# Optimization experiments

Measured on AMD Instinct MI355X. Metric: run time of the kernel, lower is better.

Reference implementation:

```python
import jax, jax.numpy as jnp
import numpy as np

NUM_USERS = 100000
NUM_ITEMS = 50000
N_NODES = NUM_USERS + NUM_ITEMS
LATENT_DIM = 64
XIJ_DIM = 16
N_LAYERS = 3
NNZ = 6400000
BATCH = 8192


def setup_inputs() -> dict:
    key = jax.random.key(0)
    ks = jax.random.split(key, 12)
    return {
        "emb_user": jax.random.normal(ks[0], (NUM_USERS, LATENT_DIM), jnp.float32),
        "emb_item": jax.random.normal(ks[1], (NUM_ITEMS, LATENT_DIM), jnp.float32),
        "emb_user_xij": jax.random.normal(ks[2], (NUM_USERS, XIJ_DIM), jnp.float32),
        "emb_item_xij1": jax.random.normal(ks[3], (NUM_ITEMS, XIJ_DIM), jnp.float32),
        "emb_item_xij0": jax.random.normal(ks[4], (NUM_ITEMS, XIJ_DIM), jnp.float32),
        "w_user": jax.random.normal(ks[5], (1,), jnp.float32),
        "w_item": jax.random.normal(ks[6], (1,), jnp.float32),
        "graph_vals": jax.random.uniform(ks[7], (NNZ,), jnp.float32),
        "graph_rows": jax.random.randint(ks[8], (NNZ,), 0, N_NODES, jnp.int64).astype(jnp.int32),
        "graph_cols": jax.random.randint(ks[9], (NNZ,), 0, N_NODES, jnp.int64).astype(jnp.int32),
        "users": jax.random.randint(ks[10], (BATCH,), 0, NUM_USERS, jnp.int64).astype(jnp.int32),
        "items": jax.random.randint(ks[11], (BATCH,), 0, NUM_ITEMS, jnp.int64).astype(jnp.int32),
        "xij": jax.random.randint(jax.random.fold_in(key, 99), (BATCH,), 0, 2, jnp.int32),
    }


def _spmm(rows, cols, vals, x):
    # y[r] = sum_{e: rows[e]==r} vals[e] * x[cols[e]]
    return jax.ops.segment_sum(vals[:, None] * x[cols], rows, num_segments=N_NODES)


def reference(emb_user, emb_item, emb_user_xij, emb_item_xij1, emb_item_xij0,
              w_user, w_item, graph_vals, graph_rows, graph_cols,
              users, items, xij):
    # LightGCN propagation with running-mean accumulator (fuses the stack+mean)
    all_emb = jnp.concatenate([emb_user, emb_item], axis=0)  # [N, D]
    acc = all_emb
    for _ in range(N_LAYERS):
        all_emb = _spmm(graph_rows, graph_cols, graph_vals, all_emb)
        acc = acc + all_emb
    light_out = acc / (N_LAYERS + 1)
    all_users = light_out[:NUM_USERS]
    all_items = light_out[NUM_USERS:]

    users_emb = w_user * all_users[users]          # [B, D]
    items_emb = w_item * all_items[items]          # [B, D]
    xij_user_emb = emb_user_xij[users]             # [B, Dx]
    xij_item_emb = jnp.where(xij[:, None].astype(bool),
                             emb_item_xij1[items], emb_item_xij0[items])

    users_mix = jax.nn.softmax(jnp.concatenate([users_emb, xij_user_emb], axis=1), axis=1)
    items_mix = jax.nn.sigmoid(jnp.concatenate([items_emb, xij_item_emb], axis=1))
    gamma = jnp.sum(users_mix * items_mix, axis=1)  # [B]
    return gamma
```

## Files before the change

kernel.cpp:

```cpp
#include <hip/hip_runtime.h>
#include <hip/hip_bf16.h>
#include <hip/hip_fp16.h>
#include <math.h>

#define NUM_USERS 100000
#define NUM_ITEMS 50000
#define N_NODES   150000
#define DIM       64
#define VAL_SCALE 16383.0f
#define VAL_INV   (1.0f / 16383.0f)

#define SSHIFT 9
#define SROWS  512
#define NBS    ((N_NODES + SROWS - 1) / SROWS)
#define CAP    16
#define FLUSH  8
#define SCAT_WGS 1280
#define GPAD   16
#define SLOTS  32768
#define PKSLOTS 22744
#define SENTINEL 0xFFFFFFFFu

__global__ void copy_init_kernel(const float4* __restrict__ eu, const float4* __restrict__ ei,
                                 ushort4* __restrict__ cur, int total4) {
    int i = blockIdx.x * blockDim.x + threadIdx.x;
    if (i >= total4) return;
    const int user_lim = NUM_USERS * (DIM / 4);
    float4 v = (i < user_lim) ? eu[i] : ei[i - user_lim];
    ushort4 h;
    h.x = __half_as_ushort(__float2half_rn(v.x));
    h.y = __half_as_ushort(__float2half_rn(v.y));
    h.z = __half_as_ushort(__float2half_rn(v.z));
    h.w = __half_as_ushort(__float2half_rn(v.w));
    cur[i] = h;
}

__global__ void gcur_init_kernel(int* __restrict__ gcur) {
    int b = blockIdx.x * blockDim.x + threadIdx.x;
    if (b < NBS) gcur[b * GPAD] = b * SLOTS;
}

__global__ __launch_bounds__(256) void binned_scatter_kernel(
        const int* __restrict__ rows, const int* __restrict__ cols,
        const float* __restrict__ vals, int* __restrict__ gcur,
        uint2* __restrict__ pk8, int nnz) {
    __shared__ unsigned       lbufA[NBS * CAP];
    __shared__ unsigned short lbufB[NBS * CAP];
    __shared__ int            lcur[NBS];
    int t = threadIdx.x;
    for (int i = t; i < NBS; i += 256) lcur[i] = 0;
    __syncthreads();

    int per_wg = (nnz + gridDim.x - 1) / gridDim.x;
    int e0 = blockIdx.x * per_wg;
    int e1 = min(e0 + per_wg, nnz);

    for (int base = e0; base < e1; base += 512) {
        #pragma unroll
        for (int k = 0; k < 2; ++k) {
            int e = base + k * 256 + t;
            if (e < e1) {
                int r = rows[e];
                unsigned q = __float2uint_rn(vals[e] * VAL_SCALE);
                unsigned ax = (unsigned)cols[e] | (q << 18);
                int b = r >> SSHIFT;
                int pos = atomicAdd(&lcur[b], 1);
                if (pos < CAP) {
                    lbufA[b * CAP + pos] = ax;
                    lbufB[b * CAP + pos] = (unsigned short)(r - (b << SSHIFT));
                } else {
                    atomicSub(&lcur[b], 1);
                    int p = atomicAdd(&gcur[b * GPAD], 8);
                    pk8[p] = make_uint2(ax, (unsigned)r);
                    #pragma unroll
                    for (int j = 1; j < 8; ++j) pk8[p + j] = make_uint2(0u, SENTINEL);
                }
            }
        }
        __syncthreads();
        for (int b2 = t; b2 < NBS; b2 += 256) {
            int c = lcur[b2];
            if (c >= FLUSH) {
                int ng = c >> 3;
                int p = atomicAdd(&gcur[b2 * GPAD], ng * 8);
                unsigned rbase = (unsigned)(b2 << SSHIFT);
                for (int j = 0; j < ng * 8; ++j)
                    pk8[p + j] = make_uint2(lbufA[b2 * CAP + j], rbase + lbufB[b2 * CAP + j]);
                int rem = c - ng * 8;
                for (int j = 0; j < rem; ++j) {
                    lbufA[b2 * CAP + j] = lbufA[b2 * CAP + ng * 8 + j];
                    lbufB[b2 * CAP + j] = lbufB[b2 * CAP + ng * 8 + j];
                }
                lcur[b2] = rem;
            }
        }
        __syncthreads();
    }
    for (int b2 = t; b2 < NBS; b2 += 256) {
        int c = lcur[b2];
        if (c > 0) {
            int p = atomicAdd(&gcur[b2 * GPAD], 8);
            unsigned rbase = (unsigned)(b2 << SSHIFT);
            for (int j = 0; j < c; ++j)
                pk8[p + j] = make_uint2(lbufA[b2 * CAP + j], rbase + lbufB[b2 * CAP + j]);
            for (int j = c; j < 8; ++j) pk8[p + j] = make_uint2(0u, SENTINEL);
        }
    }
}

__global__ __launch_bounds__(256) void bucket_build_kernel(const int* __restrict__ gcur,
                                                           const uint2* __restrict__ pk8,
                                                           unsigned* __restrict__ pk,
                                                           int* __restrict__ rowbeg,
                                                           int* __restrict__ rowend) {
    __shared__ int lc[SROWS];
    __shared__ int ps[256];
    int b  = blockIdx.x;
    int r0 = b * SROWS;
    int nr = min(r0 + SROWS, N_NODES) - r0;
    int t  = threadIdx.x;
    lc[t] = 0; lc[t + 256] = 0;
    __syncthreads();
    int s0 = b * SLOTS;
    int s1 = gcur[b * GPAD];
    for (int i = s0 + t; i < s1; i += 256) {
        uint2 en = pk8[i];
        if (en.y != SENTINEL) atomicAdd(&lc[(int)en.y - r0], 1);
    }
    __syncthreads();
    int c0 = lc[2 * t], c1 = lc[2 * t + 1];
    int pair = c0 + c1;
    ps[t] = pair;
    __syncthreads();
    #pragma unroll
    for (int off = 1; off < 256; off <<= 1) {
        int u = (t >= off) ? ps[t - off] : 0;
        __syncthreads();
        ps[t] += u;
        __syncthreads();
    }
    int base = b * PKSLOTS + ps[t] - pair;
    if (2 * t < nr)     { rowbeg[r0 + 2 * t]     = base;      rowend[r0 + 2 * t]     = base + c0; }
    if (2 * t + 1 < nr) { rowbeg[r0 + 2 * t + 1] = base + c0; rowend[r0 + 2 * t + 1] = base + c0 + c1; }
    lc[2 * t] = base;
    lc[2 * t + 1] = base + c0;
    __syncthreads();
    for (int i = s0 + t; i < s1; i += 256) {
        uint2 en = pk8[i];
        if (en.y != SENTINEL) {
            int p = atomicAdd(&lc[(int)en.y - r0], 1);
            pk[p] = en.x;
        }
    }
}

__global__ __launch_bounds__(256) void pull_kernel(const int* __restrict__ rowbeg,
                                                   const int* __restrict__ rowend,
                                                   const unsigned* __restrict__ pk,
                                                   const __half* __restrict__ x,
                                                   __half* __restrict__ y) {
    int lane = threadIdx.x & 63;
    int wv   = __builtin_amdgcn_readfirstlane(threadIdx.x >> 6);
    int row  = blockIdx.x * 4 + wv;
    if (row >= N_NODES) return;
    int s0 = rowbeg[row];
    int s1 = rowend[row];
    float acc = 0.f;
    int e = s0;
    for (; e + 8 <= s1; e += 8) {
        unsigned p0 = pk[e + 0], p1 = pk[e + 1], p2 = pk[e + 2], p3 = pk[e + 3];
        unsigned p4 = pk[e + 4], p5 = pk[e + 5], p6 = pk[e + 6], p7 = pk[e + 7];
        float x0 = __half2float(x[((p0 & 0x3FFFFu) << 6) + lane]);
        float x1 = __half2float(x[((p1 & 0x3FFFFu) << 6) + lane]);
        float x2 = __half2float(x[((p2 & 0x3FFFFu) << 6) + lane]);
        float x3 = __half2float(x[((p3 & 0x3FFFFu) << 6) + lane]);
        float x4 = __half2float(x[((p4 & 0x3FFFFu) << 6) + lane]);
        float x5 = __half2float(x[((p5 & 0x3FFFFu) << 6) + lane]);
        float x6 = __half2float(x[((p6 & 0x3FFFFu) << 6) + lane]);
        float x7 = __half2float(x[((p7 & 0x3FFFFu) << 6) + lane]);
        acc = fmaf((float)(p0 >> 18), x0, acc);
        acc = fmaf((float)(p1 >> 18), x1, acc);
        acc = fmaf((float)(p2 >> 18), x2, acc);
        acc = fmaf((float)(p3 >> 18), x3, acc);
        acc = fmaf((float)(p4 >> 18), x4, acc);
        acc = fmaf((float)(p5 >> 18), x5, acc);
        acc = fmaf((float)(p6 >> 18), x6, acc);
        acc = fmaf((float)(p7 >> 18), x7, acc);
    }
    for (; e < s1; ++e) {
        unsigned p = pk[e];
        acc = fmaf((float)(p >> 18), __half2float(x[((p & 0x3FFFFu) << 6) + lane]), acc);
    }
    y[((size_t)row << 6) + lane] = __float2half_rn(acc * VAL_INV);
}

__global__ __launch_bounds__(256) void pull_batch_kernel(const int* __restrict__ rowbeg,
                                                         const int* __restrict__ rowend,
                                                         const unsigned* __restrict__ pk,
                                                         const __half* __restrict__ x,
                                                         const int* __restrict__ users,
                                                         const int* __restrict__ items,
                                                         float* __restrict__ acc_c, int batch) {
    int lane = threadIdx.x & 63;
    int wv   = blockIdx.x * 4 + __builtin_amdgcn_readfirstlane(threadIdx.x >> 6);
    if (wv >= 2 * batch) return;
    int row = (wv < batch) ? users[wv] : NUM_USERS + items[wv - batch];
    int s0 = rowbeg[row];
    int s1 = rowend[row];
    float acc = 0.f;
    int e = s0;
    for (; e + 8 <= s1; e += 8) {
        unsigned p0 = pk[e + 0], p1 = pk[e + 1], p2 = pk[e + 2], p3 = pk[e + 3];
        unsigned p4 = pk[e + 4], p5 = pk[e + 5], p6 = pk[e + 6], p7 = pk[e + 7];
        float x0 = __half2float(x[((p0 & 0x3FFFFu) << 6) + lane]);
        float x1 = __half2float(x[((p1 & 0x3FFFFu) << 6) + lane]);
        float x2 = __half2float(x[((p2 & 0x3FFFFu) << 6) + lane]);
        float x3 = __half2float(x[((p3 & 0x3FFFFu) << 6) + lane]);
        float x4 = __half2float(x[((p4 & 0x3FFFFu) << 6) + lane]);
        float x5 = __half2float(x[((p5 & 0x3FFFFu) << 6) + lane]);
        float x6 = __half2float(x[((p6 & 0x3FFFFu) << 6) + lane]);
        float x7 = __half2float(x[((p7 & 0x3FFFFu) << 6) + lane]);
        acc = fmaf((float)(p0 >> 18), x0, acc);
        acc = fmaf((float)(p1 >> 18), x1, acc);
        acc = fmaf((float)(p2 >> 18), x2, acc);
        acc = fmaf((float)(p3 >> 18), x3, acc);
        acc = fmaf((float)(p4 >> 18), x4, acc);
        acc = fmaf((float)(p5 >> 18), x5, acc);
        acc = fmaf((float)(p6 >> 18), x6, acc);
        acc = fmaf((float)(p7 >> 18), x7, acc);
    }
    for (; e < s1; ++e) {
        unsigned p = pk[e];
        acc = fmaf((float)(p >> 18), __half2float(x[((p & 0x3FFFFu) << 6) + lane]), acc);
    }
    acc_c[((size_t)wv << 6) + lane] += acc * VAL_INV;
}

__global__ void acc_init_kernel(const float* __restrict__ eu, const float* __restrict__ ei,
                                const int* __restrict__ users, const int* __restrict__ items,
                                float* __restrict__ acc_c, int batch) {
    int gid = blockIdx.x * blockDim.x + threadIdx.x;
    int j = gid >> 6, lane = gid & 63;
    if (j >= 2 * batch) return;
    int row = (j < batch) ? users[j] : NUM_USERS + items[j - batch];
    float v = (row < NUM_USERS) ? eu[((size_t)row << 6) + lane]
                                : ei[((size_t)(row - NUM_USERS) << 6) + lane];
    acc_c[((size_t)j << 6) + lane] = v;
}

__global__ void acc_add_kernel(const __half* __restrict__ y, const int* __restrict__ users,
                               const int* __restrict__ items, float* __restrict__ acc_c,
                               int batch) {
    int gid = blockIdx.x * blockDim.x + threadIdx.x;
    int j = gid >> 6, lane = gid & 63;
    if (j >= 2 * batch) return;
    int row = (j < batch) ? users[j] : NUM_USERS + items[j - batch];
    acc_c[((size_t)j << 6) + lane] += __half2float(y[((size_t)row << 6) + lane]);
}

__global__ void final_kernel(const float* __restrict__ acc_c,
                             const float* __restrict__ exu,
                             const float* __restrict__ exi1,
                             const float* __restrict__ exi0,
                             const float* __restrict__ w_user,
                             const float* __restrict__ w_item,
                             const int* __restrict__ users,
                             const int* __restrict__ items,
                             const int* __restrict__ xijf,
                             float* __restrict__ out, int batch) {
    int gid = blockIdx.x * blockDim.x + threadIdx.x;
    int wave = gid >> 6;
    int lane = threadIdx.x & 63;
    if (wave >= batch) return;

    int u  = users[wave];
    int it = items[wave];
    int xf = xijf[wave];
    float wu = w_user[0] * 0.25f;
    float wi = w_item[0] * 0.25f;

    float ua = wu * acc_c[((size_t)wave << 6) + lane];
    float ia = wi * acc_c[((size_t)(batch + wave) << 6) + lane];
    float ub = -INFINITY, ib = 0.f;
    if (lane < 16) {
        ub = exu[(size_t)u * 16 + lane];
        ib = xf ? exi1[(size_t)it * 16 + lane] : exi0[(size_t)it * 16 + lane];
    }

    float m = fmaxf(ua, ub);
    #pragma unroll
    for (int off = 32; off; off >>= 1) m = fmaxf(m, __shfl_xor(m, off));
    float ea = expf(ua - m);
    float eb = (lane < 16) ? expf(ub - m) : 0.f;
    float s = ea + eb;
    #pragma unroll
    for (int off = 32; off; off >>= 1) s += __shfl_xor(s, off);
    float inv = 1.f / s;

    float sa = 1.f / (1.f + expf(-ia));
    float sb = (lane < 16) ? 1.f / (1.f + expf(-ib)) : 0.f;

    float g = ea * inv * sa + eb * inv * sb;
    #pragma unroll
    for (int off = 32; off; off >>= 1) g += __shfl_xor(g, off);
    if (lane == 0) out[wave] = g;
}

extern "C" void kernel_launch(void* const* d_in, const int* in_sizes, int n_in,
                              void* d_out, int out_size, void* d_ws, size_t ws_size,
                              hipStream_t stream) {
    const float* emb_user = (const float*)d_in[0];
    const float* emb_item = (const float*)d_in[1];
    const float* exu      = (const float*)d_in[2];
    const float* exi1     = (const float*)d_in[3];
    const float* exi0     = (const float*)d_in[4];
    const float* w_user   = (const float*)d_in[5];
    const float* w_item   = (const float*)d_in[6];
    const float* gvals    = (const float*)d_in[7];
    const int*   grows    = (const int*)d_in[8];
    const int*   gcols    = (const int*)d_in[9];
    const int*   users    = (const int*)d_in[10];
    const int*   items    = (const int*)d_in[11];
    const int*   xijf     = (const int*)d_in[12];
    float*       out      = (float*)d_out;

    const int nnz   = in_sizes[7];
    const int batch = in_sizes[10];

    const size_t node_elems = (size_t)N_NODES * DIM;
    const size_t PK8_BYTES  = (size_t)NBS * SLOTS * 8;
    char* w = (char*)d_ws;
    uint2*    pk8   = (uint2*)w;
    __half*   cur   = (__half*)w;
    __half*   nxt   = cur + node_elems;
    float*    acc_c = (float*)(w + 2 * node_elems * sizeof(__half));
    w += PK8_BYTES;
    unsigned* pk     = (unsigned*)w;              w += (size_t)NBS * PKSLOTS * 4;
    int*      rowbeg = (int*)w;                   w += (size_t)N_NODES * 4;
    int*      rowend = (int*)w;                   w += (size_t)N_NODES * 4;
    int*      gcur   = (int*)w;                   w += (size_t)NBS * GPAD * 4;

    const int tb = 256;
    const int total4 = N_NODES * (DIM / 4);

    gcur_init_kernel<<<(NBS + tb - 1) / tb, tb, 0, stream>>>(gcur);
    binned_scatter_kernel<<<SCAT_WGS, 256, 0, stream>>>(grows, gcols, gvals, gcur, pk8, nnz);
    bucket_build_kernel<<<NBS, 256, 0, stream>>>(gcur, pk8, pk, rowbeg, rowend);

    copy_init_kernel<<<(total4 + tb - 1) / tb, tb, 0, stream>>>(
        (const float4*)emb_user, (const float4*)emb_item, (ushort4*)cur, total4);
    acc_init_kernel<<<(2 * batch * DIM + tb - 1) / tb, tb, 0, stream>>>(
        emb_user, emb_item, users, items, acc_c, batch);

    const int pull_blocks = (N_NODES + 3) / 4;
    const int pb_blocks   = (2 * batch + 3) / 4;
    const int accb = (2 * batch * DIM + tb - 1) / tb;

    pull_kernel<<<pull_blocks, tb, 0, stream>>>(rowbeg, rowend, pk, cur, nxt);
    acc_add_kernel<<<accb, tb, 0, stream>>>(nxt, users, items, acc_c, batch);
    pull_kernel<<<pull_blocks, tb, 0, stream>>>(rowbeg, rowend, pk, nxt, cur);
    acc_add_kernel<<<accb, tb, 0, stream>>>(cur, users, items, acc_c, batch);
    pull_batch_kernel<<<pb_blocks, tb, 0, stream>>>(
        rowbeg, rowend, pk, cur, users, items, acc_c, batch);

    final_kernel<<<(batch * 64 + tb - 1) / tb, tb, 0, stream>>>(
        acc_c, exu, exi1, exi0, w_user, w_item, users, items, xijf, out, batch);
}
```

Baseline: 590.3 us.

## Vectorize pull gathers with 4-edge lane groups and widen bucket build

```diff
diff --git a/kernel.cpp b/kernel.cpp
--- a/kernel.cpp
+++ b/kernel.cpp
@@ -20,6 +20,7 @@
 #define SLOTS  32768
 #define PKSLOTS 22744
 #define SENTINEL 0xFFFFFFFFu
+#define BBT 512
 
 __global__ void copy_init_kernel(const float4* __restrict__ eu, const float4* __restrict__ ei,
                                  ushort4* __restrict__ cur, int total4) {
@@ -108,50 +109,61 @@
     }
 }
 
-__global__ __launch_bounds__(256) void bucket_build_kernel(const int* __restrict__ gcur,
+__global__ __launch_bounds__(BBT) void bucket_build_kernel(const int* __restrict__ gcur,
                                                            const uint2* __restrict__ pk8,
                                                            unsigned* __restrict__ pk,
                                                            int* __restrict__ rowbeg,
                                                            int* __restrict__ rowend) {
     __shared__ int lc[SROWS];
-    __shared__ int ps[256];
+    __shared__ int ps[SROWS];
     int b  = blockIdx.x;
     int r0 = b * SROWS;
     int nr = min(r0 + SROWS, N_NODES) - r0;
     int t  = threadIdx.x;
-    lc[t] = 0; lc[t + 256] = 0;
+    lc[t] = 0;
     __syncthreads();
-    int s0 = b * SLOTS;
-    int s1 = gcur[b * GPAD];
-    for (int i = s0 + t; i < s1; i += 256) {
-        uint2 en = pk8[i];
-        if (en.y != SENTINEL) atomicAdd(&lc[(int)en.y - r0], 1);
-    }
+
+    const uint4* p4 = (const uint4*)pk8;
+    int i0   = (b * SLOTS) >> 1;
+    int iend = gcur[b * GPAD] >> 1;
+
+    #define CNT(q) { \
+        if ((q).y != SENTINEL) atomicAdd(&lc[(int)(q).y - r0], 1); \
+        if ((q).w != SENTINEL) atomicAdd(&lc[(int)(q).w - r0], 1); }
+
+    int i = i0 + t;
+    for (; i + 3 * BBT < iend; i += 4 * BBT) {
+        uint4 qa = p4[i], qb = p4[i + BBT], qc = p4[i + 2 * BBT], qd = p4[i + 3 * BBT];
+        CNT(qa) CNT(qb) CNT(qc) CNT(qd)
+    }
+    for (; i < iend; i += BBT) { uint4 qa = p4[i]; CNT(qa) }
     __syncthreads();
-    int c0 = lc[2 * t], c1 = lc[2 * t + 1];
-    int pair = c0 + c1;
-    ps[t] = pair;
+
+    int c = lc[t];
+    ps[t] = c;
     __syncthreads();
     #pragma unroll
-    for (int off = 1; off < 256; off <<= 1) {
+    for (int off = 1; off < SROWS; off <<= 1) {
         int u = (t >= off) ? ps[t - off] : 0;
         __syncthreads();
         ps[t] += u;
         __syncthreads();
     }
-    int base = b * PKSLOTS + ps[t] - pair;
-    if (2 * t < nr)     { rowbeg[r0 + 2 * t]     = base;      rowend[r0 + 2 * t]     = base + c0; }
-    if (2 * t + 1 < nr) { rowbeg[r0 + 2 * t + 1] = base + c0; rowend[r0 + 2 * t + 1] = base + c0 + c1; }
-    lc[2 * t] = base;
-    lc[2 * t + 1] = base + c0;
+    int base = b * PKSLOTS + ps[t] - c;
+    if (t < nr) { rowbeg[r0 + t] = base; rowend[r0 + t] = base + c; }
+    lc[t] = base;
     __syncthreads();
-    for (int i = s0 + t; i < s1; i += 256) {
-        uint2 en = pk8[i];
-        if (en.y != SENTINEL) {
-            int p = atomicAdd(&lc[(int)en.y - r0], 1);
-            pk[p] = en.x;
-        }
-    }
+
+    #define PLC(q) { \
+        if ((q).y != SENTINEL) { int p_ = atomicAdd(&lc[(int)(q).y - r0], 1); pk[p_] = (q).x; } \
+        if ((q).w != SENTINEL) { int p_ = atomicAdd(&lc[(int)(q).w - r0], 1); pk[p_] = (q).z; } }
+
+    i = i0 + t;
+    for (; i + 3 * BBT < iend; i += 4 * BBT) {
+        uint4 qa = p4[i], qb = p4[i + BBT], qc = p4[i + 2 * BBT], qd = p4[i + 3 * BBT];
+        PLC(qa) PLC(qb) PLC(qc) PLC(qd)
+    }
+    for (; i < iend; i += BBT) { uint4 qa = p4[i]; PLC(qa) }
 }
 
 __global__ __launch_bounds__(256) void pull_kernel(const int* __restrict__ rowbeg,
@@ -163,35 +175,49 @@
     int wv   = __builtin_amdgcn_readfirstlane(threadIdx.x >> 6);
     int row  = blockIdx.x * 4 + wv;
     if (row >= N_NODES) return;
+    int g  = lane >> 4;
+    int dl = lane & 15;
     int s0 = rowbeg[row];
     int s1 = rowend[row];
-    float acc = 0.f;
+    float a0 = 0.f, a1 = 0.f, a2 = 0.f, a3 = 0.f;
     int e = s0;
     for (; e + 8 <= s1; e += 8) {
-        unsigned p0 = pk[e + 0], p1 = pk[e + 1], p2 = pk[e + 2], p3 = pk[e + 3];
-        unsigned p4 = pk[e + 4], p5 = pk[e + 5], p6 = pk[e + 6], p7 = pk[e + 7];
-        float x0 = __half2float(x[((p0 & 0x3FFFFu) << 6) + lane]);
-        float x1 = __half2float(x[((p1 & 0x3FFFFu) << 6) + lane]);
-        float x2 = __half2float(x[((p2 & 0x3FFFFu) << 6) + lane]);
-        float x3 = __half2float(x[((p3 & 0x3FFFFu) << 6) + lane]);
-        float x4 = __half2float(x[((p4 & 0x3FFFFu) << 6) + lane]);
-        float x5 = __half2float(x[((p5 & 0x3FFFFu) << 6) + lane]);
-        float x6 = __half2float(x[((p6 & 0x3FFFFu) << 6) + lane]);
-        float x7 = __half2float(x[((p7 & 0x3FFFFu) << 6) + lane]);
-        acc = fmaf((float)(p0 >> 18), x0, acc);
-        acc = fmaf((float)(p1 >> 18), x1, acc);
-        acc = fmaf((float)(p2 >> 18), x2, acc);
-        acc = fmaf((float)(p3 >> 18), x3, acc);
-        acc = fmaf((float)(p4 >> 18), x4, acc);
-        acc = fmaf((float)(p5 >> 18), x5, acc);
-        acc = fmaf((float)(p6 >> 18), x6, acc);
-        acc = fmaf((float)(p7 >> 18), x7, acc);
-    }
-    for (; e < s1; ++e) {
-        unsigned p = pk[e];
-        acc = fmaf((float)(p >> 18), __half2float(x[((p & 0x3FFFFu) << 6) + lane]), acc);
-    }
-    y[((size_t)row << 6) + lane] = __float2half_rn(acc * VAL_INV);
+        unsigned pa = pk[e + g];
+        unsigned pb = pk[e + 4 + g];
+        const ushort4 ha = *(const ushort4*)(x + (((pa & 0x3FFFFu) << 6) + (dl << 2)));
+        const ushort4 hb = *(const ushort4*)(x + (((pb & 0x3FFFFu) << 6) + (dl << 2)));
+        float wa = (float)(pa >> 18), wb = (float)(pb >> 18);
+        a0 = fmaf(wa, __half2float(__ushort_as_half(ha.x)), a0);
+        a1 = fmaf(wa, __half2float(__ushort_as_half(ha.y)), a1);
+        a2 = fmaf(wa, __half2float(__ushort_as_half(ha.z)), a2);
+        a3 = fmaf(wa, __half2float(__ushort_as_half(ha.w)), a3);
+        a0 = fmaf(wb, __half2float(__ushort_as_half(hb.x)), a0);
+        a1 = fmaf(wb, __half2float(__ushort_as_half(hb.y)), a1);
+        a2 = fmaf(wb, __half2float(__ushort_as_half(hb.z)), a2);
+        a3 = fmaf(wb, __half2float(__ushort_as_half(hb.w)), a3);
+    }
+    for (; e < s1; e += 4) {
+        int ee = e + g;
+        unsigned p = (ee < s1) ? pk[ee] : 0u;
+        const ushort4 h = *(const ushort4*)(x + (((p & 0x3FFFFu) << 6) + (dl << 2)));
+        float w = (float)(p >> 18);
+        a0 = fmaf(w, __half2float(__ushort_as_half(h.x)), a0);
+        a1 = fmaf(w, __half2float(__ushort_as_half(h.y)), a1);
+        a2 = fmaf(w, __half2float(__ushort_as_half(h.z)), a2);
+        a3 = fmaf(w, __half2float(__ushort_as_half(h.w)), a3);
+    }
+    a0 += __shfl_xor(a0, 16); a0 += __shfl_xor(a0, 32);
+    a1 += __shfl_xor(a1, 16); a1 += __shfl_xor(a1, 32);
+    a2 += __shfl_xor(a2, 16); a2 += __shfl_xor(a2, 32);
+    a3 += __shfl_xor(a3, 16); a3 += __shfl_xor(a3, 32);
+    if (lane < 16) {
+        ushort4 hv;
+        hv.x = __half_as_ushort(__float2half_rn(a0 * VAL_INV));
+        hv.y = __half_as_ushort(__float2half_rn(a1 * VAL_INV));
+        hv.z = __half_as_ushort(__float2half_rn(a2 * VAL_INV));
+        hv.w = __half_as_ushort(__float2half_rn(a3 * VAL_INV));
+        *(ushort4*)(y + (((size_t)row << 6) + (dl << 2))) = hv;
+    }
 }
 
 __global__ __launch_bounds__(256) void pull_batch_kernel(const int* __restrict__ rowbeg,
@@ -205,35 +231,50 @@
     int wv   = blockIdx.x * 4 + __builtin_amdgcn_readfirstlane(threadIdx.x >> 6);
     if (wv >= 2 * batch) return;
     int row = (wv < batch) ? users[wv] : NUM_USERS + items[wv - batch];
+    int g  = lane >> 4;
+    int dl = lane & 15;
     int s0 = rowbeg[row];
     int s1 = rowend[row];
-    float acc = 0.f;
+    float a0 = 0.f, a1 = 0.f, a2 = 0.f, a3 = 0.f;
     int e = s0;
     for (; e + 8 <= s1; e += 8) {
-        unsigned p0 = pk[e + 0], p1 = pk[e + 1], p2 = pk[e + 2], p3 = pk[e + 3];
-        unsigned p4 = pk[e + 4], p5 = pk[e + 5], p6 = pk[e + 6], p7 = pk[e + 7];
-        float x0 = __half2float(x[((p0 & 0x3FFFFu) << 6) + lane]);
-        float x1 = __half2float(x[((p1 & 0x3FFFFu) << 6) + lane]);
-        float x2 = __half2float(x[((p2 & 0x3FFFFu) << 6) + lane]);
-        float x3 = __half2float(x[((p3 & 0x3FFFFu) << 6) + lane]);
-        float x4 = __half2float(x[((p4 & 0x3FFFFu) << 6) + lane]);
-        float x5 = __half2float(x[((p5 & 0x3FFFFu) << 6) + lane]);
-        float x6 = __half2float(x[((p6 & 0x3FFFFu) << 6) + lane]);
-        float x7 = __half2float(x[((p7 & 0x3FFFFu) << 6) + lane]);
-        acc = fmaf((float)(p0 >> 18), x0, acc);
-        acc = fmaf((float)(p1 >> 18), x1, acc);
-        acc = fmaf((float)(p2 >> 18), x2, acc);
-        acc = fmaf((float)(p3 >> 18), x3, acc);
-        acc = fmaf((float)(p4 >> 18), x4, acc);
-        acc = fmaf((float)(p5 >> 18), x5, acc);
-        acc = fmaf((float)(p6 >> 18), x6, acc);
-        acc = fmaf((float)(p7 >> 18), x7, acc);
-    }
-    for (; e < s1; ++e) {
-        unsigned p = pk[e];
-        acc = fmaf((float)(p >> 18), __half2float(x[((p & 0x3FFFFu) << 6) + lane]), acc);
-    }
-    acc_c[((size_t)wv << 6) + lane] += acc * VAL_INV;
+        unsigned pa = pk[e + g];
+        unsigned pb = pk[e + 4 + g];
+        const ushort4 ha = *(const ushort4*)(x + (((pa & 0x3FFFFu) << 6) + (dl << 2)));
+        const ushort4 hb = *(const ushort4*)(x + (((pb & 0x3FFFFu) << 6) + (dl << 2)));
+        float wa = (float)(pa >> 18), wb = (float)(pb >> 18);
+        a0 = fmaf(wa, __half2float(__ushort_as_half(ha.x)), a0);
+        a1 = fmaf(wa, __half2float(__ushort_as_half(ha.y)), a1);
+        a2 = fmaf(wa, __half2float(__ushort_as_half(ha.z)), a2);
+        a3 = fmaf(wa, __half2float(__ushort_as_half(ha.w)), a3);
+        a0 = fmaf(wb, __half2float(__ushort_as_half(hb.x)), a0);
+        a1 = fmaf(wb, __half2float(__ushort_as_half(hb.y)), a1);
+        a2 = fmaf(wb, __half2float(__ushort_as_half(hb.z)), a2);
+        a3 = fmaf(wb, __half2float(__ushort_as_half(hb.w)), a3);
+    }
+    for (; e < s1; e += 4) {
+        int ee = e + g;
+        unsigned p = (ee < s1) ? pk[ee] : 0u;
+        const ushort4 h = *(const ushort4*)(x + (((p & 0x3FFFFu) << 6) + (dl << 2)));
+        float w = (float)(p >> 18);
+        a0 = fmaf(w, __half2float(__ushort_as_half(h.x)), a0);
+        a1 = fmaf(w, __half2float(__ushort_as_half(h.y)), a1);
+        a2 = fmaf(w, __half2float(__ushort_as_half(h.z)), a2);
+        a3 = fmaf(w, __half2float(__ushort_as_half(h.w)), a3);
+    }
+    a0 += __shfl_xor(a0, 16); a0 += __shfl_xor(a0, 32);
+    a1 += __shfl_xor(a1, 16); a1 += __shfl_xor(a1, 32);
+    a2 += __shfl_xor(a2, 16); a2 += __shfl_xor(a2, 32);
+    a3 += __shfl_xor(a3, 16); a3 += __shfl_xor(a3, 32);
+    if (lane < 16) {
+        float4* dst = (float4*)(acc_c + (((size_t)wv << 6) + (dl << 2)));
+        float4 v = *dst;
+        v.x += a0 * VAL_INV;
+        v.y += a1 * VAL_INV;
+        v.z += a2 * VAL_INV;
+        v.w += a3 * VAL_INV;
+        *dst = v;
+    }
 }
 
 __global__ void acc_init_kernel(const float* __restrict__ eu, const float* __restrict__ ei,
@@ -345,7 +386,7 @@
 
     gcur_init_kernel<<<(NBS + tb - 1) / tb, tb, 0, stream>>>(gcur);
     binned_scatter_kernel<<<SCAT_WGS, 256, 0, stream>>>(grows, gcols, gvals, gcur, pk8, nnz);
-    bucket_build_kernel<<<NBS, 256, 0, stream>>>(gcur, pk8, pk, rowbeg, rowend);
+    bucket_build_kernel<<<NBS, BBT, 0, stream>>>(gcur, pk8, pk, rowbeg, rowend);
 
     copy_init_kernel<<<(total4 + tb - 1) / tb, tb, 0, stream>>>(
         (const float4*)emb_user, (const float4*)emb_item, (ushort4*)cur, total4);
```

Result: faster. 569.2 us (-3.6%).
